# Optimization experiments

Measured on AMD Instinct MI355X. Metric: run time of the kernel, lower is better.

The kernel has to match this reference:

```python
import jax, jax.numpy as jnp
import numpy as np

FEAT = 256          # feat_channels == point_feat_channels == in_channels
STACK = 3           # stacked_convs
NPTS = 9            # num_points -> dcn_kernel = 3
NCLS = 80           # num_classes
GM = 0.1            # gradient_mul
GROUPS = 32         # 32 * 256 // 256
EPS = 1e-5
BIAS_CLS = -float(np.log((1 - 0.01) / 0.01))  # prior_prob focal-bias init


def conv2d(x, w, b=None):
    y = jax.lax.conv_general_dilated(x, w, (1, 1), 'SAME',
                                     dimension_numbers=('NCHW', 'OIHW', 'NCHW'))
    return y if b is None else y + b[None, :, None, None]


def group_norm(x, w, b):
    B, C, H, W = x.shape
    xg = x.reshape(B, GROUPS, C // GROUPS, H, W)
    mu = xg.mean((2, 3, 4), keepdims=True)
    var = xg.var((2, 3, 4), keepdims=True)
    xn = ((xg - mu) * jax.lax.rsqrt(var + EPS)).reshape(B, C, H, W)
    return xn * w[None, :, None, None] + b[None, :, None, None]


def bilinear_sample(x, py, px):
    # x: [B,C,H,W]; py,px: [B,K,H,W] absolute sample coords -> [B,C,K,H,W]
    B, C, H, W = x.shape
    y0 = jnp.floor(py); x0 = jnp.floor(px)
    wy = (py - y0)[:, None]; wx = (px - x0)[:, None]  # [B,1,K,H,W]
    xf = x.reshape(B, C, H * W)

    def gather(yi, xi):
        valid = (yi >= 0) & (yi < H) & (xi >= 0) & (xi < W)
        yic = jnp.clip(yi, 0, H - 1).astype(jnp.int32)
        xic = jnp.clip(xi, 0, W - 1).astype(jnp.int32)
        idx = (yic * W + xic).reshape(B, -1)                       # [B,K*H*W]
        g = jax.vmap(lambda xb, ib: xb[:, ib])(xf, idx)            # [B,C,K*H*W]
        g = g.reshape(B, C, *yi.shape[1:])
        return g * valid[:, None].astype(x.dtype)

    v00 = gather(y0, x0); v01 = gather(y0, x0 + 1)
    v10 = gather(y0 + 1, x0); v11 = gather(y0 + 1, x0 + 1)
    return (v00 * (1 - wy) * (1 - wx) + v01 * (1 - wy) * wx
            + v10 * wy * (1 - wx) + v11 * wy * wx)


def deform_conv(x, offset, w):
    # x: [B,C,H,W]; offset: [B,2K,H,W] as (dy,dx) per kernel point; w: [O,C,kh,kw]
    B, C, H, W = x.shape
    O, _, kh, kw = w.shape
    K = kh * kw
    off = offset.reshape(B, K, 2, H, W)
    by = jnp.repeat(jnp.arange(kh) - (kh - 1) // 2, kw).astype(x.dtype)  # [K]
    bx = jnp.tile(jnp.arange(kw) - (kw - 1) // 2, kh).astype(x.dtype)
    gy = jnp.arange(H, dtype=x.dtype)[None, None, :, None]
    gx = jnp.arange(W, dtype=x.dtype)[None, None, None, :]
    py = gy + by[None, :, None, None] + off[:, :, 0]  # [B,K,H,W]
    px = gx + bx[None, :, None, None] + off[:, :, 1]
    sampled = bilinear_sample(x, py, px)              # [B,C,K,H,W]
    return jnp.einsum('bckhw,ock->bohw', sampled, w.reshape(O, C, K))


def dcn_base_offset():
    base = np.arange(-1, 2, dtype=np.float32)
    y = np.repeat(base, 3); x = np.tile(base, 3)
    return jnp.asarray(np.stack([y, x], axis=1).reshape(1, -1, 1, 1))  # [1,18,1,1]


def setup_inputs() -> dict:
    key = jax.random.key(0)
    ks = jax.random.split(key, 10)
    std = 0.01
    d = {}
    d['features'] = jax.random.normal(ks[0], (4, FEAT, 64, 64), jnp.float32)
    d['cls_w'] = std * jax.random.normal(ks[1], (STACK, FEAT, FEAT, 3, 3), jnp.float32)
    d['reg_w'] = std * jax.random.normal(ks[2], (STACK, FEAT, FEAT, 3, 3), jnp.float32)
    d['cls_gn_w'] = jnp.ones((STACK, FEAT), jnp.float32)
    d['cls_gn_b'] = jnp.zeros((STACK, FEAT), jnp.float32)
    d['reg_gn_w'] = jnp.ones((STACK, FEAT), jnp.float32)
    d['reg_gn_b'] = jnp.zeros((STACK, FEAT), jnp.float32)
    d['init_conv_w'] = std * jax.random.normal(ks[3], (FEAT, FEAT, 3, 3), jnp.float32)
    d['init_conv_b'] = jnp.zeros((FEAT,), jnp.float32)
    d['init_out_w'] = std * jax.random.normal(ks[4], (2 * NPTS, FEAT, 1, 1), jnp.float32)
    d['init_out_b'] = jnp.zeros((2 * NPTS,), jnp.float32)
    d['cls_dcn_w'] = std * jax.random.normal(ks[5], (FEAT, FEAT, 3, 3), jnp.float32)
    d['cls_out_w'] = std * jax.random.normal(ks[6], (NCLS, FEAT, 1, 1), jnp.float32)
    d['cls_out_b'] = jnp.full((NCLS,), BIAS_CLS, jnp.float32)
    d['ref_dcn_w'] = std * jax.random.normal(ks[7], (FEAT, FEAT, 3, 3), jnp.float32)
    d['ref_out_w'] = std * jax.random.normal(ks[8], (2 * NPTS, FEAT, 1, 1), jnp.float32)
    d['ref_out_b'] = jnp.zeros((2 * NPTS,), jnp.float32)
    return d


def reference(features, cls_w, reg_w, cls_gn_w, cls_gn_b, reg_gn_w, reg_gn_b,
              init_conv_w, init_conv_b, init_out_w, init_out_b,
              cls_dcn_w, cls_out_w, cls_out_b,
              ref_dcn_w, ref_out_w, ref_out_b):
    cls_feat = reg_feat = features
    for i in range(STACK):
        cls_feat = jax.nn.relu(group_norm(conv2d(cls_feat, cls_w[i]), cls_gn_w[i], cls_gn_b[i]))
        reg_feat = jax.nn.relu(group_norm(conv2d(reg_feat, reg_w[i]), reg_gn_w[i], reg_gn_b[i]))
    pts_init = conv2d(jax.nn.relu(conv2d(reg_feat, init_conv_w, init_conv_b)),
                      init_out_w, init_out_b)                     # [B,18,H,W]
    pts_gm = (1.0 - GM) * jax.lax.stop_gradient(pts_init) + GM * pts_init
    dcn_offset = pts_gm - dcn_base_offset()  # DeformConv adds base back internally
    cls_out = conv2d(jax.nn.relu(deform_conv(cls_feat, dcn_offset, cls_dcn_w)),
                     cls_out_w, cls_out_b)                        # [B,80,H,W]
    pts_refine = conv2d(jax.nn.relu(deform_conv(reg_feat, dcn_offset, ref_dcn_w)),
                        ref_out_w, ref_out_b) + jax.lax.stop_gradient(pts_init)
    # outputs concatenated along channels: [cls(80) | pts_init(18) | pts_refine(18)]
    return jnp.concatenate([cls_out, pts_init, pts_refine], axis=1)
```

## Files before the change

### kernel.cpp

```cpp
#include <hip/hip_runtime.h>

typedef unsigned short u16;
typedef unsigned char u8;
typedef __attribute__((ext_vector_type(8))) short short8;
typedef __attribute__((ext_vector_type(4))) float floatx4;
typedef __attribute__((ext_vector_type(2))) float floatx2;
typedef __attribute__((ext_vector_type(2))) long longx2;

#define MTOT    16384
#define PADIMG  (66 * 66)
#define PADELEM (4 * PADIMG * 256)
#define PADB    ((size_t)PADELEM * 2)
#define WSTEP   (256 * 2304)

__device__ __forceinline__ float bf2f(u16 u) {
  union { unsigned int i; float f; } c; c.i = ((unsigned int)u) << 16; return c.f;
}
__device__ __forceinline__ u16 f2bf(float f) {
  union { float f; unsigned int i; } c; c.f = f;
  unsigned int r = c.i + 0x7FFFu + ((c.i >> 16) & 1u);
  return (u16)(r >> 16);
}

__device__ __forceinline__ void gl_lds16(const void* g, void* l) {
  __builtin_amdgcn_global_load_lds(
      (const __attribute__((address_space(1))) void*)g,
      (__attribute__((address_space(3))) void*)l, 16, 0, 0);
}

__device__ __forceinline__ int lds_slot32(int row, int q) {
  return row * 32 + ((q ^ ((row >> 1) & 3)) << 3);
}
__device__ __forceinline__ int lds_slot64(int row, int q) {
  return row * 64 + ((q ^ (row & 7)) << 3);
}
__device__ __forceinline__ int lds_slot8r(int row, int quad) {
  return row * 64 + ((quad ^ ((row >> 1) & 3)) << 4);
}
__device__ __forceinline__ int permw(int w) {
  return ((w >> 3) & 3) * 16 + ((w >> 5) & 1) * 8 + (w & 7);
}

__global__ void setup_all(const float* __restrict__ cls_w, const float* __restrict__ reg_w,
                          const float* __restrict__ initw, const float* __restrict__ clsd,
                          const float* __restrict__ refd,
                          const float* __restrict__ iw, const float* __restrict__ cw,
                          const float* __restrict__ rw,
                          const float* __restrict__ features,
                          u16* __restrict__ dst3, u16* __restrict__ dst1,
                          u8* __restrict__ pads8, u8* __restrict__ wf8,
                          u16* __restrict__ padbf) {
  int blk = blockIdx.x;
  int t = threadIdx.x;
  if (blk < 2304) {
    int w = blk >> 8;
    int o = blk & 255;
    const float* src = (w < 3) ? cls_w + (size_t)w * WSTEP
                     : (w < 6) ? reg_w + (size_t)(w - 3) * WSTEP
                     : (w == 6) ? initw : (w == 7) ? clsd : refd;
    __shared__ float wl[2304];
    const float* so = src + (size_t)o * 2304;
    #pragma unroll
    for (int p = 0; p < 9; ++p) wl[p * 256 + t] = so[p * 256 + t];
    __syncthreads();
    if (w == 6) {
      u16* dw = dst3 + (size_t)o * 2304;
      #pragma unroll
      for (int p = 0; p < 9; ++p)
        dw[p * 256 + t] = f2bf(wl[t * 9 + p]);
    } else if (t < 128) {
      int slot = (w < 6) ? w : (w - 1);
      u8* dw8 = wf8 + (size_t)slot * WSTEP + (size_t)o * 2304;
      int c = 2 * t;
      int pos = (c & 192) + permw(c & 63);
      #pragma unroll
      for (int p = 0; p < 9; ++p) {
        float f0 = wl[c * 9 + p] * 64.f;
        float f1 = wl[(c + 1) * 9 + p] * 64.f;
        int pk = __builtin_amdgcn_cvt_pk_fp8_f32(f0, f1, 0, false);
        *(u16*)(dw8 + p * 256 + pos) = (u16)(pk & 0xFFFF);
      }
    }
  } else if (blk < 2688) {
    int bb = blk - 2304;
    int wsel = bb >> 7;
    const float* src = wsel == 0 ? iw : wsel == 1 ? cw : rw;
    int nvalid = wsel == 1 ? 80 : 18;
    float scale = wsel == 0 ? 1.f : (1.f / 64.f);
    int idx = (bb & 127) * 256 + t;
    int o = idx >> 8, c = idx & 255;
    dst1[(size_t)wsel * 32768 + idx] = f2bf(o < nvalid ? src[o * 256 + c] * scale : 0.f);
  } else if (blk < 3712) {
    __shared__ float tile[64][65];
    int bb = blk - 2688;
    int c0 = (bb & 3) * 64;
    int y  = (bb >> 2) & 63;
    int b  = bb >> 8;
    #pragma unroll
    for (int i = 0; i < 16; ++i) {
      int lin = t + i * 256; int c = lin >> 6, x = lin & 63;
      tile[c][x] = features[((b * 256 + c0 + c) * 64 + y) * 64 + x];
    }
    __syncthreads();
    #pragma unroll
    for (int i = 0; i < 8; ++i) {
      int lin = t + i * 256;
      int x = lin >> 5, c2 = lin & 31;
      int pk = __builtin_amdgcn_cvt_pk_fp8_f32(tile[2 * c2][x], tile[2 * c2 + 1][x], 0, false);
      *(u16*)(pads8 + (size_t)((b * 66 + y + 1) * 66 + (x + 1)) * 256
              + c0 + permw(2 * c2)) = (u16)pk;
    }
  } else if (blk < 5012) {
    int idx = (blk - 3712) * 256 + t;
    int c4 = (idx & 63) << 2;
    int r = idx >> 6;
    int pix = r % 260;
    int ib = r / 260;
    int y, x;
    if (pix < 66)       { y = 0;  x = pix; }
    else if (pix < 132) { y = 65; x = pix - 66; }
    else if (pix < 196) { y = pix - 132 + 1; x = 0; }
    else                { y = pix - 196 + 1; x = 65; }
    size_t o = (((size_t)ib * PADIMG) + y * 66 + x) * 256 + c4;
    *(unsigned int*)(pads8 + o) = 0u;
  } else {
    int idx = (blk - 5012) * 256 + t;
    int c4 = (idx & 63) << 2;
    int r = idx >> 6;
    int pix = r % 260;
    int b = r / 260;
    int y, x;
    if (pix < 66)       { y = 0;  x = pix; }
    else if (pix < 132) { y = 65; x = pix - 66; }
    else if (pix < 196) { y = pix - 132 + 1; x = 0; }
    else                { y = pix - 196 + 1; x = 65; }
    size_t o = (((size_t)b * PADIMG) + y * 66 + x) * 256 + c4;
    *(ushort4*)(padbf + o) = (ushort4){0, 0, 0, 0};
  }
}

__global__ void __launch_bounds__(256)
gn_apply2(const u16* __restrict__ stage, const float2* __restrict__ st,
          const float* __restrict__ gwc, const float* __restrict__ gbc,
          const float* __restrict__ gwr, const float* __restrict__ gbr,
          u8* __restrict__ cdst8, u8* __restrict__ rdst8, u16* __restrict__ rbf) {
  int tid = blockIdx.x * 256 + threadIdx.x;
  int tower = tid >> 20;
  int r = tid & 0xFFFFF;
  int m = r >> 6, c4 = (r & 63) << 2;
  ushort4 u = *(const ushort4*)(stage + ((size_t)tower << 22) + (size_t)m * 256 + c4);
  int b = m >> 12, p = m & 4095, y = p >> 6, x = p & 63;
  float2 ss = st[tower * 128 + b * 32 + (c4 >> 3)];
  float mu = ss.x * (1.f / 32768.f);
  float var = ss.y * (1.f / 32768.f) - mu * mu;
  float rinv = rsqrtf(var + 1e-5f);
  const float* gw = tower ? gwr : gwc;
  const float* gb = tower ? gbr : gbc;
  float v0 = fmaxf((bf2f(u.x) - mu) * rinv * gw[c4 + 0] + gb[c4 + 0], 0.f);
  float v1 = fmaxf((bf2f(u.y) - mu) * rinv * gw[c4 + 1] + gb[c4 + 1], 0.f);
  float v2 = fmaxf((bf2f(u.z) - mu) * rinv * gw[c4 + 2] + gb[c4 + 2], 0.f);
  float v3 = fmaxf((bf2f(u.w) - mu) * rinv * gw[c4 + 3] + gb[c4 + 3], 0.f);
  size_t pixbase = (size_t)((b * 66 + y + 1) * 66 + (x + 1)) * 256;
  int pk = __builtin_amdgcn_cvt_pk_fp8_f32(v0, v1, 0, false);
  pk = __builtin_amdgcn_cvt_pk_fp8_f32(v2, v3, pk, true);
  *(int*)((tower ? rdst8 : cdst8) + pixbase + (c4 & 192) + permw(c4 & 63)) = pk;
  if (tower && rbf) {
    ushort4 o;
    o.x = f2bf(v0); o.y = f2bf(v1); o.z = f2bf(v2); o.w = f2bf(v3);
    *(ushort4*)(rbf + pixbase + c4) = o;
  }
}

__global__ void __launch_bounds__(256)
dcn_sample2(const u8* __restrict__ featC, const u8* __restrict__ featR,
            const float* __restrict__ pts,
            u8* __restrict__ AC, u8* __restrict__ AR) {
  int blk = blockIdx.x;
  const u8* featpad = blk < 1024 ? featC : featR;
  u8* A = blk < 1024 ? AC : AR;
  int mblk = blk & 1023;
  int t = threadIdx.x;
  int m = mblk * 16 + (t >> 4);
  int l = t & 15;
  int b = m >> 12, p = m & 4095, y = p >> 6, x = p & 63;
  const float* pp = pts + (size_t)m * 18;
  const u8* fb = featpad + (size_t)b * PADIMG * 256 + l * 4;
  u8* am = A + (size_t)m * 2304 + l * 4;
  #pragma unroll
  for (int kk = 0; kk < 9; ++kk) {
    float py = (float)y + pp[2 * kk];
    float px = (float)x + pp[2 * kk + 1];
    float fy = floorf(py), fx = floorf(px);
    int y0 = (int)fy, x0 = (int)fx;
    float wy = py - fy, wx = px - fx;
    float w00 = (1.f - wy) * (1.f - wx), w01 = (1.f - wy) * wx;
    float w10 = wy * (1.f - wx), w11 = wy * wx;
    bool yok0 = (unsigned)y0 < 64u, yok1 = (unsigned)(y0 + 1) < 64u;
    bool xok0 = (unsigned)x0 < 64u, xok1 = (unsigned)(x0 + 1) < 64u;
    const u8* base = fb + ((y0 + 1) * 66 + (x0 + 1)) * 256;
    float r[16];
    #pragma unroll
    for (int i = 0; i < 16; ++i) r[i] = 0.f;
    #define ACCUM(OFF, W) { \
      _Pragma("unroll") \
      for (int c = 0; c < 4; ++c) { \
        unsigned int v = *(const unsigned int*)(base + (OFF) + c * 64); \
        floatx2 lo = __builtin_amdgcn_cvt_pk_f32_fp8(v, false); \
        floatx2 hi = __builtin_amdgcn_cvt_pk_f32_fp8(v, true); \
        r[c*4+0] += (W) * lo.x; r[c*4+1] += (W) * lo.y; \
        r[c*4+2] += (W) * hi.x; r[c*4+3] += (W) * hi.y; } }
    if (yok0 & xok0) ACCUM(0, w00)
    if (yok0 & xok1) ACCUM(256, w01)
    if (yok1 & xok0) ACCUM(66 * 256, w10)
    if (yok1 & xok1) ACCUM(67 * 256, w11)
    #undef ACCUM
    #pragma unroll
    for (int c = 0; c < 4; ++c) {
      int pk = __builtin_amdgcn_cvt_pk_fp8_f32(r[c*4+0], r[c*4+1], 0, false);
      pk = __builtin_amdgcn_cvt_pk_fp8_f32(r[c*4+2], r[c*4+3], pk, true);
      *(int*)(am + kk * 256 + c * 64) = pk;
    }
  }
}

template <int AMODE, int EP, int KSZ, int BN, int BK, int NPAIR, int FP8 = 0>
__global__ void __launch_bounds__(256)
gemm_kernel(const u16* __restrict__ A0, const u16* __restrict__ A1,
            const u16* __restrict__ W0, const u16* __restrict__ W1,
            const float* __restrict__ bias0, const float* __restrict__ bias1,
            u16* __restrict__ outb0, u16* __restrict__ outb1,
            float2* __restrict__ st0, float2* __restrict__ st1,
            float* __restrict__ outf,
            const float* __restrict__ addpts0, const float* __restrict__ addpts1,
            float* __restrict__ ptsout0, float* __restrict__ ptsout1,
            int nv0, int nv1, int cb0, int cb1) {
  constexpr int NJ = BN / 32;
  __shared__ __align__(16) u16 As[128 * BK];
  __shared__ __align__(16) u16 Bs[BN * BK];
  int t = threadIdx.x;
  int blk = blockIdx.x;
  int pair = 0;
  if constexpr (NPAIR == 2) { pair = blk & 1; blk >>= 1; }
  const u16* A        = pair ? A1 : A0;
  const u16* Wp       = pair ? W1 : W0;
  const float* bias   = pair ? bias1 : bias0;
  u16* outb           = pair ? outb1 : outb0;
  float2* st          = pair ? st1 : st0;
  const float* addpts = pair ? addpts1 : addpts0;
  float* ptsout       = pair ? ptsout1 : ptsout0;
  int nv = pair ? nv1 : nv0;
  int cb = pair ? cb1 : cb0;

  int bm = blk & 127, bn = blk >> 7;
  int lane = t & 63, wave = t >> 6;
  int wm = (wave & 1) << 6;
  int wn = (wave >> 1) * (BN / 2);
  int quad = lane >> 4, r16 = lane & 15;

  floatx4 acc[4][NJ];
  #pragma unroll
  for (int i = 0; i < 4; ++i)
    #pragma unroll
    for (int j = 0; j < NJ; ++j)
      acc[i][j] = (floatx4){0.f, 0.f, 0.f, 0.f};

  if constexpr (FP8 == 1) {
    u8* As8 = (u8*)As;
    u8* Bs8 = (u8*)Bs;
    const u8* A8 = (const u8*)A;
    const u8* W8 = (const u8*)Wp;
    int row = t >> 2;
    int cq = (t & 3) ^ ((t >> 3) & 3);
    int m0 = bm * 128 + row, m1 = m0 + 64;
    int abase0, abase1;
    if constexpr (AMODE == 1) {
      int b0 = m0 >> 12, p0 = m0 & 4095;
      int b1 = m1 >> 12, p1 = m1 & 4095;
      abase0 = ((b0 * 66 + (p0 >> 6)) * 66 + (p0 & 63)) * 256 + cq * 16;
      abase1 = ((b1 * 66 + (p1 >> 6)) * 66 + (p1 & 63)) * 256 + cq * 16;
    } else {
      abase0 = m0 * KSZ + cq * 16;
      abase1 = m1 * KSZ + cq * 16;
    }
    const u8* wg8 = W8 + (size_t)(bn * BN + row) * KSZ + cq * 16;

    for (int s = 0; s < KSZ / 64; ++s) {
      int d;
      if constexpr (AMODE == 1) {
        int kk = s >> 2;
        int c0 = (s & 3) << 6;
        int ky = kk / 3, kx = kk - ky * 3;
        d = ((ky * 66 + kx) << 8) + c0;
      } else {
        d = s * 64;
      }
      gl_lds16(A8 + abase0 + d, As8 + t * 16);
      gl_lds16(A8 + abase1 + d, As8 + 4096 + t * 16);
      gl_lds16(wg8 + s * 64, Bs8 + t * 16);
      __syncthreads();
      long af8[2][4], bf8[2][NJ];
      #pragma unroll
      for (int i = 0; i < 4; ++i) {
        longx2 v = *(const longx2*)&As8[lds_slot8r(wm + i * 16 + r16, quad)];
        af8[0][i] = v.x; af8[1][i] = v.y;
      }
      #pragma unroll
      for (int j = 0; j < NJ; ++j) {
        longx2 v = *(const longx2*)&Bs8[lds_slot8r(wn + j * 16 + r16, quad)];
        bf8[0][j] = v.x; bf8[1][j] = v.y;
      }
      #pragma unroll
      for (int ks = 0; ks < 2; ++ks)
        #pragma unroll
        for (int i = 0; i < 4; ++i)
          #pragma unroll
          for (int j = 0; j < NJ; ++j)
            acc[i][j] = __builtin_amdgcn_mfma_f32_16x16x32_fp8_fp8(af8[ks][i], bf8[ks][j], acc[i][j], 0, 0, 0);
      __syncthreads();
    }
  } else if constexpr (BK == 64) {
    int sub = t >> 3;
    int cq = (t & 7) ^ (sub & 7);
    int abase[4];
    #pragma unroll
    for (int k = 0; k < 4; ++k) {
      int m = bm * 128 + k * 32 + sub;
      if constexpr (AMODE == 1) {
        int b = m >> 12, p = m & 4095;
        abase[k] = ((b * 66 + (p >> 6)) * 66 + (p & 63)) * 256 + cq * 8;
      } else {
        abase[k] = m * KSZ + cq * 8;
      }
    }
    const u16* wg = Wp + (size_t)(bn * BN + sub) * KSZ + cq * 8;

    for (int s = 0; s < KSZ / 64; ++s) {
      int d;
      if constexpr (AMODE == 1) {
        int kk = s >> 2;
        int c0 = (s & 3) << 6;
        int ky = kk / 3, kx = kk - ky * 3;
        d = ((ky * 66 + kx) << 8) + c0;
      } else {
        d = s * 64;
      }
      #pragma unroll
      for (int k = 0; k < 4; ++k)
        gl_lds16(A + abase[k] + d, &As[k * 2048 + t * 8]);
      #pragma unroll
      for (int k = 0; k < BN / 32; ++k)
        gl_lds16(wg + (size_t)(k * 32) * KSZ + s * 64, &Bs[k * 2048 + t * 8]);
      __syncthreads();
      short8 af[2][4], bfr[2][NJ];
      #pragma unroll
      for (int ks = 0; ks < 2; ++ks) {
        #pragma unroll
        for (int i = 0; i < 4; ++i)
          af[ks][i] = *(const short8*)&As[lds_slot64(wm + i * 16 + r16, ks * 4 + quad)];
        #pragma unroll
        for (int j = 0; j < NJ; ++j)
          bfr[ks][j] = *(const short8*)&Bs[lds_slot64(wn + j * 16 + r16, ks * 4 + quad)];
      }
      #pragma unroll
      for (int ks = 0; ks < 2; ++ks)
        #pragma unroll
        for (int i = 0; i < 4; ++i)
          #pragma unroll
          for (int j = 0; j < NJ; ++j)
            acc[i][j] = __builtin_amdgcn_mfma_f32_16x16x32_bf16(af[ks][i], bfr[ks][j], acc[i][j], 0, 0, 0);
      __syncthreads();
    }
  } else {
    int row = t >> 2;
    int chunkS = (t & 3) ^ ((t >> 3) & 3);
    int m0 = bm * 128 + row, m1 = m0 + 64;
    int abase0, abase1;
    if constexpr (AMODE == 1) {
      int b0 = m0 >> 12, p0 = m0 & 4095;
      int b1 = m1 >> 12, p1 = m1 & 4095;
      abase0 = ((b0 * 66 + (p0 >> 6)) * 66 + (p0 & 63)) * 256 + chunkS * 8;
      abase1 = ((b1 * 66 + (p1 >> 6)) * 66 + (p1 & 63)) * 256 + chunkS * 8;
    } else {
      abase0 = m0 * KSZ + chunkS * 8;
      abase1 = m1 * KSZ + chunkS * 8;
    }
    const u16* wg = Wp + (size_t)(bn * BN + row) * KSZ + chunkS * 8;

    for (int s = 0; s < KSZ / 32; ++s) {
      int d;
      if constexpr (AMODE == 1) {
        int kk = s >> 3;
        int c0 = (s & 7) << 5;
        int ky = kk / 3, kx = kk - ky * 3;
        d = ((ky * 66 + kx) << 8) + c0;
      } else {
        d = s * 32;
      }
      gl_lds16(A + abase0 + d, &As[t * 8]);
      gl_lds16(A + abase1 + d, &As[2048 + t * 8]);
      gl_lds16(wg + s * 32, &Bs[t * 8]);
      if constexpr (BN == 128)
        gl_lds16(wg + (size_t)64 * KSZ + s * 32, &Bs[2048 + t * 8]);
      __syncthreads();
      short8 af[4], bfr[NJ];
      #pragma unroll
      for (int i = 0; i < 4; ++i)
        af[i] = *(const short8*)&As[lds_slot32(wm + i * 16 + r16, quad)];
      #pragma unroll
      for (int j = 0; j < NJ; ++j)
        bfr[j] = *(const short8*)&Bs[lds_slot32(wn + j * 16 + r16, quad)];
      #pragma unroll
      for (int i = 0; i < 4; ++i)
        #pragma unroll
        for (int j = 0; j < NJ; ++j)
          acc[i][j] = __builtin_amdgcn_mfma_f32_16x16x32_bf16(af[i], bfr[j], acc[i][j], 0, 0, 0);
      __syncthreads();
    }
  }

  #pragma unroll
  for (int j = 0; j < NJ; ++j) {
    int gn = bn * BN + wn + j * 16 + r16;
    float s = 0.f, s2 = 0.f;
    #pragma unroll
    for (int i = 0; i < 4; ++i) {
      #pragma unroll
      for (int r = 0; r < 4; ++r) {
        int gm = bm * 128 + wm + i * 16 + quad * 4 + r;
        float v = acc[i][j][r];
        if constexpr (EP == 0) {
          outb[(size_t)gm * 256 + gn] = f2bf(v);
          s += v; s2 += v * v;
        } else if constexpr (EP == 1) {
          outb[(size_t)gm * 256 + gn] = f2bf(fmaxf(v + bias[gn], 0.f));
        } else if constexpr (EP == 2) {
          outb[(size_t)gm * 256 + gn] = f2bf(fmaxf(v, 0.f));
        } else {
          if (gn < nv) {
            v += bias[gn];
            if (addpts) v += addpts[(size_t)gm * 18 + gn];
            if (ptsout) ptsout[(size_t)gm * 18 + gn] = v;
            int bb = gm >> 12, p = gm & 4095;
            outf[(size_t)((bb * 116 + cb + gn) << 12) + p] = v;
          }
        }
      }
    }
    if constexpr (EP == 0) {
      s += __shfl_xor(s, 1);  s2 += __shfl_xor(s2, 1);
      s += __shfl_xor(s, 2);  s2 += __shfl_xor(s2, 2);
      s += __shfl_xor(s, 4);  s2 += __shfl_xor(s2, 4);
      s += __shfl_xor(s, 16); s2 += __shfl_xor(s2, 16);
      s += __shfl_xor(s, 32); s2 += __shfl_xor(s2, 32);
      if ((lane & 55) == 0) {
        float2* sp = st + ((bm >> 5) * 32) + (gn >> 3);
        atomicAdd(&sp->x, s);
        atomicAdd(&sp->y, s2);
      }
    }
  }
}

extern "C" void kernel_launch(void* const* d_in, const int* in_sizes, int n_in,
                              void* d_out, int out_size, void* d_ws, size_t ws_size,
                              hipStream_t stream) {
  (void)in_sizes; (void)n_in; (void)out_size;
  const float* features    = (const float*)d_in[0];
  const float* cls_w       = (const float*)d_in[1];
  const float* reg_w       = (const float*)d_in[2];
  const float* cls_gn_w    = (const float*)d_in[3];
  const float* cls_gn_b    = (const float*)d_in[4];
  const float* reg_gn_w    = (const float*)d_in[5];
  const float* reg_gn_b    = (const float*)d_in[6];
  const float* init_conv_w = (const float*)d_in[7];
  const float* init_conv_b = (const float*)d_in[8];
  const float* init_out_w  = (const float*)d_in[9];
  const float* init_out_b  = (const float*)d_in[10];
  const float* cls_dcn_w   = (const float*)d_in[11];
  const float* cls_out_w   = (const float*)d_in[12];
  const float* cls_out_b   = (const float*)d_in[13];
  const float* ref_dcn_w   = (const float*)d_in[14];
  const float* ref_out_w   = (const float*)d_in[15];
  const float* ref_out_b   = (const float*)d_in[16];
  float* out = (float*)d_out;

  char* ws = (char*)d_ws;
  size_t off = 0;
  auto alloc = [&](size_t bytes) {
    char* p = ws + off;
    off += (bytes + 255) & ~(size_t)255;
    return p;
  };
  u16* wbf        = (u16*)alloc((size_t)WSTEP * 2);
  u8*  wf8        = (u8*)alloc((size_t)8 * WSTEP);
  u16* w1         = (u16*)alloc((size_t)3 * 32768 * 2);
  u8* xpad8       = (u8*)alloc(PADELEM);
  u8* cpadA8      = (u8*)alloc(PADELEM);
  u8* cpadB8      = (u8*)alloc(PADELEM);
  u8* rpadA8      = (u8*)alloc(PADELEM);
  u8* rpadB8      = (u8*)alloc(PADELEM);
  u16* rpadBF     = (u16*)alloc(PADB);
  float* ptsbuf   = (float*)alloc((size_t)MTOT * 18 * 4);
  float2* statsAll= (float2*)alloc(3 * 256 * sizeof(float2));
  u16* initf      = (u16*)alloc((size_t)MTOT * 256 * 2);
  u16* dcnout     = (u16*)alloc((size_t)2 * MTOT * 256 * 2);
  char* unionReg  = alloc((size_t)MTOT * 2304);
  u16* cstage     = (u16*)unionReg;
  u8* adcn        = (u8*)unionReg;
  u8* adcn2       = (u8*)alloc((size_t)MTOT * 2304);
  bool paired_dcn = (off <= ws_size);

  (void)hipMemsetAsync(statsAll, 0, 3 * 256 * sizeof(float2), stream);
  setup_all<<<5272, 256, 0, stream>>>(cls_w, reg_w, init_conv_w, cls_dcn_w, ref_dcn_w,
                                      init_out_w, cls_out_w, ref_out_w, features,
                                      wbf, w1, xpad8, wf8, rpadBF);

  const u8* curC = xpad8; const u8* curR = xpad8;
  u8* nxtC = cpadA8; u8* altC = cpadB8;
  u8* nxtR = rpadA8; u8* altR = rpadB8;
  for (int i = 0; i < 3; ++i) {
    gemm_kernel<1, 0, 2304, 64, 64, 2, 1><<<1024, 256, 0, stream>>>(
        (const u16*)curC, (const u16*)curR,
        (const u16*)(wf8 + (size_t)i * WSTEP), (const u16*)(wf8 + (size_t)(3 + i) * WSTEP),
        nullptr, nullptr, cstage, cstage + (size_t)MTOT * 256,
        statsAll + i * 256, statsAll + i * 256 + 128,
        nullptr, nullptr, nullptr, nullptr, nullptr, 0, 0, 0, 0);
    gn_apply2<<<8192, 256, 0, stream>>>(cstage, statsAll + i * 256,
        cls_gn_w + i * 256, cls_gn_b + i * 256, reg_gn_w + i * 256, reg_gn_b + i * 256,
        nxtC, nxtR, (i == 2) ? rpadBF : nullptr);
    curC = nxtC; { u8* tmp = nxtC; nxtC = altC; altC = tmp; }
    curR = nxtR; { u8* tmp = nxtR; nxtR = altR; altR = tmp; }
  }
  const u8* cls_feat8 = curC;
  const u8* reg_feat8 = curR;

  gemm_kernel<1, 1, 2304, 32, 64, 1><<<1024, 256, 0, stream>>>(
      rpadBF, nullptr, wbf, nullptr,
      init_conv_b, nullptr, initf, nullptr, nullptr, nullptr,
      nullptr, nullptr, nullptr, nullptr, nullptr, 0, 0, 0, 0);
  gemm_kernel<0, 3, 256, 64, 32, 1><<<256, 256, 0, stream>>>(
      initf, nullptr, w1, nullptr, init_out_b, nullptr,
      nullptr, nullptr, nullptr, nullptr, out,
      nullptr, nullptr, ptsbuf, nullptr, 18, 0, 80, 0);

  if (paired_dcn) {
    dcn_sample2<<<2048, 256, 0, stream>>>(cls_feat8, reg_feat8, ptsbuf, adcn, adcn2);
    gemm_kernel<0, 2, 2304, 64, 64, 2, 1><<<1024, 256, 0, stream>>>(
        (const u16*)adcn, (const u16*)adcn2,
        (const u16*)(wf8 + (size_t)6 * WSTEP), (const u16*)(wf8 + (size_t)7 * WSTEP),
        nullptr, nullptr, dcnout, dcnout + (size_t)MTOT * 256, nullptr, nullptr,
        nullptr, nullptr, nullptr, nullptr, nullptr, 0, 0, 0, 0);
  } else {
    dcn_sample2<<<1024, 256, 0, stream>>>(cls_feat8, cls_feat8, ptsbuf, adcn, adcn);
    gemm_kernel<0, 2, 2304, 64, 64, 1, 1><<<512, 256, 0, stream>>>(
        (const u16*)adcn, nullptr, (const u16*)(wf8 + (size_t)6 * WSTEP), nullptr,
        nullptr, nullptr, dcnout, nullptr, nullptr, nullptr,
        nullptr, nullptr, nullptr, nullptr, nullptr, 0, 0, 0, 0);
    dcn_sample2<<<1024, 256, 0, stream>>>(reg_feat8, reg_feat8, ptsbuf, adcn, adcn);
    gemm_kernel<0, 2, 2304, 64, 64, 1, 1><<<512, 256, 0, stream>>>(
        (const u16*)adcn, nullptr, (const u16*)(wf8 + (size_t)7 * WSTEP), nullptr,
        nullptr, nullptr, dcnout + (size_t)MTOT * 256, nullptr, nullptr, nullptr,
        nullptr, nullptr, nullptr, nullptr, nullptr, 0, 0, 0, 0);
  }

  gemm_kernel<0, 3, 256, 64, 32, 2><<<512, 256, 0, stream>>>(
      dcnout, dcnout + (size_t)MTOT * 256, w1 + 32768, w1 + 2 * 32768,
      cls_out_b, ref_out_b, nullptr, nullptr, nullptr, nullptr, out,
      nullptr, ptsbuf, nullptr, nullptr, 80, 18, 0, 98);
}
```

Measured before the change: 378.1 us.

## Use fp8 for tower conv staging and init conv, drop bf16 padded copy

The stacked-conv GEMM epilogue now writes its pre-norm staging output as fp8 instead of bf16, and the group-norm apply kernel reads fp8. The init 3x3 conv now runs as an fp8 GEMM on the existing fp8 reg feature map with fp8-packed weights and a 1/64 rescale. This removes the separate bf16 padded reg-feature buffer, its border zeroing, and the bf16 weight conversion. It halves staging and init-conv traffic but lowers precision of the pre-norm activations and of the point offsets that feed the deformable sampling.

```diff
diff --git a/kernel.cpp b/kernel.cpp
--- a/kernel.cpp
+++ b/kernel.cpp
@@ -10,7 +10,6 @@
 #define MTOT    16384
 #define PADIMG  (66 * 66)
 #define PADELEM (4 * PADIMG * 256)
-#define PADB    ((size_t)PADELEM * 2)
 #define WSTEP   (256 * 2304)
 
 __device__ __forceinline__ float bf2f(u16 u) {
@@ -20,6 +19,9 @@
   union { float f; unsigned int i; } c; c.f = f;
   unsigned int r = c.i + 0x7FFFu + ((c.i >> 16) & 1u);
   return (u16)(r >> 16);
+}
+__device__ __forceinline__ u8 f2fp8(float f) {
+  return (u8)(__builtin_amdgcn_cvt_pk_fp8_f32(f, f, 0, false) & 0xFF);
 }
 
 __device__ __forceinline__ void gl_lds16(const void* g, void* l) {
@@ -47,9 +49,8 @@
                           const float* __restrict__ iw, const float* __restrict__ cw,
                           const float* __restrict__ rw,
                           const float* __restrict__ features,
-                          u16* __restrict__ dst3, u16* __restrict__ dst1,
-                          u8* __restrict__ pads8, u8* __restrict__ wf8,
-                          u16* __restrict__ padbf) {
+                          u16* __restrict__ dst1,
+                          u8* __restrict__ pads8, u8* __restrict__ wf8) {
   int blk = blockIdx.x;
   int t = threadIdx.x;
   if (blk < 2304) {
@@ -63,13 +64,8 @@
     #pragma unroll
     for (int p = 0; p < 9; ++p) wl[p * 256 + t] = so[p * 256 + t];
     __syncthreads();
-    if (w == 6) {
-      u16* dw = dst3 + (size_t)o * 2304;
-      #pragma unroll
-      for (int p = 0; p < 9; ++p)
-        dw[p * 256 + t] = f2bf(wl[t * 9 + p]);
-    } else if (t < 128) {
-      int slot = (w < 6) ? w : (w - 1);
+    if (t < 128) {
+      int slot = (w < 6) ? w : (w == 6) ? 8 : (w - 1);
       u8* dw8 = wf8 + (size_t)slot * WSTEP + (size_t)o * 2304;
       int c = 2 * t;
       int pos = (c & 192) + permw(c & 63);
@@ -110,7 +106,7 @@
       *(u16*)(pads8 + (size_t)((b * 66 + y + 1) * 66 + (x + 1)) * 256
               + c0 + permw(2 * c2)) = (u16)pk;
     }
-  } else if (blk < 5012) {
+  } else {
     int idx = (blk - 3712) * 256 + t;
     int c4 = (idx & 63) << 2;
     int r = idx >> 6;
@@ -123,32 +119,22 @@
     else                { y = pix - 196 + 1; x = 65; }
     size_t o = (((size_t)ib * PADIMG) + y * 66 + x) * 256 + c4;
     *(unsigned int*)(pads8 + o) = 0u;
-  } else {
-    int idx = (blk - 5012) * 256 + t;
-    int c4 = (idx & 63) << 2;
-    int r = idx >> 6;
-    int pix = r % 260;
-    int b = r / 260;
-    int y, x;
-    if (pix < 66)       { y = 0;  x = pix; }
-    else if (pix < 132) { y = 65; x = pix - 66; }
-    else if (pix < 196) { y = pix - 132 + 1; x = 0; }
-    else                { y = pix - 196 + 1; x = 65; }
-    size_t o = (((size_t)b * PADIMG) + y * 66 + x) * 256 + c4;
-    *(ushort4*)(padbf + o) = (ushort4){0, 0, 0, 0};
   }
 }
 
 __global__ void __launch_bounds__(256)
-gn_apply2(const u16* __restrict__ stage, const float2* __restrict__ st,
+gn_apply2(const u8* __restrict__ stage, const float2* __restrict__ st,
           const float* __restrict__ gwc, const float* __restrict__ gbc,
           const float* __restrict__ gwr, const float* __restrict__ gbr,
-          u8* __restrict__ cdst8, u8* __restrict__ rdst8, u16* __restrict__ rbf) {
+          u8* __restrict__ cdst8, u8* __restrict__ rdst8) {
   int tid = blockIdx.x * 256 + threadIdx.x;
   int tower = tid >> 20;
   int r = tid & 0xFFFFF;
   int m = r >> 6, c4 = (r & 63) << 2;
-  ushort4 u = *(const ushort4*)(stage + ((size_t)tower << 22) + (size_t)m * 256 + c4);
+  unsigned int v = *(const unsigned int*)(stage + ((size_t)tower << 22)
+                                          + (size_t)m * 256 + c4);
+  floatx2 lo = __builtin_amdgcn_cvt_pk_f32_fp8(v, false);
+  floatx2 hi = __builtin_amdgcn_cvt_pk_f32_fp8(v, true);
   int b = m >> 12, p = m & 4095, y = p >> 6, x = p & 63;
   float2 ss = st[tower * 128 + b * 32 + (c4 >> 3)];
   float mu = ss.x * (1.f / 32768.f);
@@ -156,19 +142,14 @@
   float rinv = rsqrtf(var + 1e-5f);
   const float* gw = tower ? gwr : gwc;
   const float* gb = tower ? gbr : gbc;
-  float v0 = fmaxf((bf2f(u.x) - mu) * rinv * gw[c4 + 0] + gb[c4 + 0], 0.f);
-  float v1 = fmaxf((bf2f(u.y) - mu) * rinv * gw[c4 + 1] + gb[c4 + 1], 0.f);
-  float v2 = fmaxf((bf2f(u.z) - mu) * rinv * gw[c4 + 2] + gb[c4 + 2], 0.f);
-  float v3 = fmaxf((bf2f(u.w) - mu) * rinv * gw[c4 + 3] + gb[c4 + 3], 0.f);
+  float v0 = fmaxf((lo.x - mu) * rinv * gw[c4 + 0] + gb[c4 + 0], 0.f);
+  float v1 = fmaxf((lo.y - mu) * rinv * gw[c4 + 1] + gb[c4 + 1], 0.f);
+  float v2 = fmaxf((hi.x - mu) * rinv * gw[c4 + 2] + gb[c4 + 2], 0.f);
+  float v3 = fmaxf((hi.y - mu) * rinv * gw[c4 + 3] + gb[c4 + 3], 0.f);
   size_t pixbase = (size_t)((b * 66 + y + 1) * 66 + (x + 1)) * 256;
   int pk = __builtin_amdgcn_cvt_pk_fp8_f32(v0, v1, 0, false);
   pk = __builtin_amdgcn_cvt_pk_fp8_f32(v2, v3, pk, true);
   *(int*)((tower ? rdst8 : cdst8) + pixbase + (c4 & 192) + permw(c4 & 63)) = pk;
-  if (tower && rbf) {
-    ushort4 o;
-    o.x = f2bf(v0); o.y = f2bf(v1); o.z = f2bf(v2); o.w = f2bf(v3);
-    *(ushort4*)(rbf + pixbase + c4) = o;
-  }
 }
 
 __global__ void __launch_bounds__(256)
@@ -296,7 +277,8 @@
       }
       gl_lds16(A8 + abase0 + d, As8 + t * 16);
       gl_lds16(A8 + abase1 + d, As8 + 4096 + t * 16);
-      gl_lds16(wg8 + s * 64, Bs8 + t * 16);
+      if (BN == 64 || t < 4 * BN)
+        gl_lds16(wg8 + s * 64, Bs8 + t * 16);
       __syncthreads();
       long af8[2][4], bf8[2][NJ];
       #pragma unroll
@@ -429,9 +411,10 @@
         int gm = bm * 128 + wm + i * 16 + quad * 4 + r;
         float v = acc[i][j][r];
         if constexpr (EP == 0) {
-          outb[(size_t)gm * 256 + gn] = f2bf(v);
+          ((u8*)outb)[(size_t)gm * 256 + gn] = f2fp8(v);
           s += v; s2 += v * v;
         } else if constexpr (EP == 1) {
+          if constexpr (FP8 == 1) v *= (1.f / 64.f);
           outb[(size_t)gm * 256 + gn] = f2bf(fmaxf(v + bias[gn], 0.f));
         } else if constexpr (EP == 2) {
           outb[(size_t)gm * 256 + gn] = f2bf(fmaxf(v, 0.f));
@@ -491,29 +474,27 @@
     off += (bytes + 255) & ~(size_t)255;
     return p;
   };
-  u16* wbf        = (u16*)alloc((size_t)WSTEP * 2);
-  u8*  wf8        = (u8*)alloc((size_t)8 * WSTEP);
+  u8*  wf8        = (u8*)alloc((size_t)9 * WSTEP);
   u16* w1         = (u16*)alloc((size_t)3 * 32768 * 2);
   u8* xpad8       = (u8*)alloc(PADELEM);
   u8* cpadA8      = (u8*)alloc(PADELEM);
   u8* cpadB8      = (u8*)alloc(PADELEM);
   u8* rpadA8      = (u8*)alloc(PADELEM);
   u8* rpadB8      = (u8*)alloc(PADELEM);
-  u16* rpadBF     = (u16*)alloc(PADB);
   float* ptsbuf   = (float*)alloc((size_t)MTOT * 18 * 4);
   float2* statsAll= (float2*)alloc(3 * 256 * sizeof(float2));
   u16* initf      = (u16*)alloc((size_t)MTOT * 256 * 2);
   u16* dcnout     = (u16*)alloc((size_t)2 * MTOT * 256 * 2);
   char* unionReg  = alloc((size_t)MTOT * 2304);
-  u16* cstage     = (u16*)unionReg;
+  u8* cstage8     = (u8*)unionReg;
   u8* adcn        = (u8*)unionReg;
   u8* adcn2       = (u8*)alloc((size_t)MTOT * 2304);
   bool paired_dcn = (off <= ws_size);
 
   (void)hipMemsetAsync(statsAll, 0, 3 * 256 * sizeof(float2), stream);
-  setup_all<<<5272, 256, 0, stream>>>(cls_w, reg_w, init_conv_w, cls_dcn_w, ref_dcn_w,
+  setup_all<<<5012, 256, 0, stream>>>(cls_w, reg_w, init_conv_w, cls_dcn_w, ref_dcn_w,
                                       init_out_w, cls_out_w, ref_out_w, features,
-                                      wbf, w1, xpad8, wf8, rpadBF);
+                                      w1, xpad8, wf8);
 
   const u8* curC = xpad8; const u8* curR = xpad8;
   u8* nxtC = cpadA8; u8* altC = cpadB8;
@@ -522,20 +503,20 @@
     gemm_kernel<1, 0, 2304, 64, 64, 2, 1><<<1024, 256, 0, stream>>>(
         (const u16*)curC, (const u16*)curR,
         (const u16*)(wf8 + (size_t)i * WSTEP), (const u16*)(wf8 + (size_t)(3 + i) * WSTEP),
-        nullptr, nullptr, cstage, cstage + (size_t)MTOT * 256,
+        nullptr, nullptr, (u16*)cstage8, (u16*)(cstage8 + (size_t)MTOT * 256),
         statsAll + i * 256, statsAll + i * 256 + 128,
         nullptr, nullptr, nullptr, nullptr, nullptr, 0, 0, 0, 0);
-    gn_apply2<<<8192, 256, 0, stream>>>(cstage, statsAll + i * 256,
+    gn_apply2<<<8192, 256, 0, stream>>>(cstage8, statsAll + i * 256,
         cls_gn_w + i * 256, cls_gn_b + i * 256, reg_gn_w + i * 256, reg_gn_b + i * 256,
-        nxtC, nxtR, (i == 2) ? rpadBF : nullptr);
+        nxtC, nxtR);
     curC = nxtC; { u8* tmp = nxtC; nxtC = altC; altC = tmp; }
     curR = nxtR; { u8* tmp = nxtR; nxtR = altR; altR = tmp; }
   }
   const u8* cls_feat8 = curC;
   const u8* reg_feat8 = curR;
 
-  gemm_kernel<1, 1, 2304, 32, 64, 1><<<1024, 256, 0, stream>>>(
-      rpadBF, nullptr, wbf, nullptr,
+  gemm_kernel<1, 1, 2304, 32, 64, 1, 1><<<1024, 256, 0, stream>>>(
+      (const u16*)reg_feat8, nullptr, (const u16*)(wf8 + (size_t)8 * WSTEP), nullptr,
       init_conv_b, nullptr, initf, nullptr, nullptr, nullptr,
       nullptr, nullptr, nullptr, nullptr, nullptr, 0, 0, 0, 0);
   gemm_kernel<0, 3, 256, 64, 32, 1><<<256, 256, 0, stream>>>(
```

New measurement: 375.2 us. About the same (-0.8%).
